# Kernel optimization log

Measured on AMD Instinct MI355X. Metric: run time of the kernel, lower is better.

## Reference

```python
import jax, jax.numpy as jnp
import numpy as np

B, CIN, COUT = 4, 64, 64
D, H, W = 8, 48, 48
KD = KH = KW = 3
K = KD * KH * KW  # 27 sampling taps
STRIDE, PAD, DIL = 1, 1, 1
KOFF, POFF = 3, 1
OFFSET_SCALE = 1.0


def setup_inputs() -> dict:
    key = jax.random.key(0)
    ks = jax.random.split(key, 7)
    x = jax.random.normal(ks[0], (B, CIN, D, H, W), jnp.float32)
    w_off = jax.random.normal(ks[1], (K * 3, CIN, KOFF, KOFF, KOFF), jnp.float32) * 0.01
    b_off = jax.random.normal(ks[2], (K * 3,), jnp.float32) * 0.01
    w_mask = jax.random.normal(ks[3], (K, CIN, KOFF, KOFF, KOFF), jnp.float32) * 0.05
    b_mask = jax.random.normal(ks[4], (K,), jnp.float32) * 0.05
    weight = jax.random.normal(ks[5], (COUT, CIN, KD, KH, KW), jnp.float32) * 0.02
    bias = jax.random.normal(ks[6], (COUT,), jnp.float32) * 0.02
    return dict(x=x, w_off=w_off, b_off=b_off, w_mask=w_mask, b_mask=b_mask,
                weight=weight, bias=bias)


def _conv3d(x, w, b, pad):
    out = jax.lax.conv_general_dilated(
        x, w, window_strides=(1, 1, 1), padding=[(pad, pad)] * 3,
        dimension_numbers=('NCDHW', 'OIDHW', 'NCDHW'))
    return out + b[None, :, None, None, None]


def _trilinear(x_flat, pz, py, px):
    # x_flat: [B, C, N]; pz/py/px: [B, N] fractional positions. Zero padding outside.
    z0, y0, x0 = jnp.floor(pz), jnp.floor(py), jnp.floor(px)
    acc = jnp.zeros_like(x_flat)
    for dz in (0.0, 1.0):
        for dy in (0.0, 1.0):
            for dx in (0.0, 1.0):
                zi, yi, xi = z0 + dz, y0 + dy, x0 + dx
                wgt = ((1.0 - jnp.abs(pz - zi)) * (1.0 - jnp.abs(py - yi))
                       * (1.0 - jnp.abs(px - xi)))
                valid = ((zi >= 0) & (zi < D) & (yi >= 0) & (yi < H)
                         & (xi >= 0) & (xi < W)).astype(x_flat.dtype)
                idx = ((jnp.clip(zi, 0, D - 1) * H + jnp.clip(yi, 0, H - 1)) * W
                       + jnp.clip(xi, 0, W - 1)).astype(jnp.int32)
                g = jnp.take_along_axis(x_flat, idx[:, None, :], axis=2)  # [B,C,N]
                acc = acc + g * (wgt * valid)[:, None, :]
    return acc


def reference(x, w_off, b_off, w_mask, b_mask, weight, bias):
    N = D * H * W
    # learned per-tap 3D offsets: [K, B, 3, N] ordered (dz, dy, dx)
    off = _conv3d(x, w_off, b_off, POFF).reshape(B, K, 3, N)
    off = jnp.transpose(off, (1, 0, 2, 3))
    # DCNv3-style attention mask: softmax over the K taps
    mask = jax.nn.softmax(_conv3d(x, w_mask, b_mask, POFF).reshape(B, K, N), axis=1)
    mask = jnp.transpose(mask, (1, 0, 2))  # [K, B, N]
    zo, yo, xo = jnp.meshgrid(jnp.arange(D, dtype=jnp.float32),
                              jnp.arange(H, dtype=jnp.float32),
                              jnp.arange(W, dtype=jnp.float32), indexing='ij')
    zo, yo, xo = zo.reshape(-1), yo.reshape(-1), xo.reshape(-1)  # [N]
    k_idx = jnp.arange(K)
    kz = (k_idx // (KH * KW)).astype(jnp.float32)
    ky = ((k_idx // KW) % KH).astype(jnp.float32)
    kx = (k_idx % KW).astype(jnp.float32)
    wk = jnp.transpose(weight.reshape(COUT, CIN, K), (2, 0, 1))  # [K, Cout, Cin]
    x_flat = x.reshape(B, CIN, N)

    def step(acc, inp):
        off_k, m_k, kzf, kyf, kxf, w_k = inp
        pz = zo[None] * STRIDE - PAD + kzf * DIL + OFFSET_SCALE * off_k[:, 0]
        py = yo[None] * STRIDE - PAD + kyf * DIL + OFFSET_SCALE * off_k[:, 1]
        px = xo[None] * STRIDE - PAD + kxf * DIL + OFFSET_SCALE * off_k[:, 2]
        s = _trilinear(x_flat, pz, py, px) * m_k[:, None, :]  # [B,Cin,N]
        return acc + jnp.einsum('oi,bin->bon', w_k, s), None

    acc0 = jnp.zeros((B, COUT, N), x.dtype)
    acc, _ = jax.lax.scan(step, acc0, (off, mask, kz, ky, kx, wk))
    return (acc + bias[None, :, None]).reshape(B, COUT, D, H, W)
```

## Files before the change

### kernel.cpp

```cpp
#include <hip/hip_runtime.h>
#include <hip/hip_bf16.h>
#include <math.h>

#define B_    4
#define CIN_  64
#define COUT_ 64
#define DD    8
#define HH    48
#define WW    48
#define HW2   (HH * WW)
#define NN    (DD * HH * WW)
#define BN    (B_ * NN)
#define KK    27
#define RS    116

typedef float f32x2 __attribute__((ext_vector_type(2)));
typedef float f32x4 __attribute__((ext_vector_type(4)));
typedef unsigned int u32x4 __attribute__((ext_vector_type(4)));
typedef __bf16 bf16x8 __attribute__((ext_vector_type(8)));
typedef __hip_bfloat16 bf16_t;

__device__ __forceinline__ float bflo(unsigned int u) {
  return __uint_as_float(u << 16);
}
__device__ __forceinline__ float bfhi(unsigned int u) {
  return __uint_as_float(u & 0xffff0000u);
}

__global__ __launch_bounds__(256) void init_kernel(
    const float* __restrict__ w_off, const float* __restrict__ w_mask,
    const float* __restrict__ weight, bf16_t* __restrict__ wB,
    bf16_t* __restrict__ wBd, bf16_t* __restrict__ zp)
{
  const int o = blockIdx.x * 256 + threadIdx.x;
  {
    const int ci = o & 63;
    const int ch = (o >> 6) % 112;
    const int k  = o / (112 * 64);
    float v = 0.f;
    if (ch < 81)       v = w_off[((size_t)ch * CIN_ + ci) * KK + k];
    else if (ch < 108) v = w_mask[((size_t)(ch - 81) * CIN_ + ci) * KK + k];
    wB[o] = __float2bfloat16(v);
  }
  if (o < KK * CIN_ * COUT_) {
    const int ci = o & 63;
    const int co = (o >> 6) & 63;
    const int k  = o >> 12;
    wBd[o] = __float2bfloat16(weight[((size_t)co * CIN_ + ci) * KK + k]);
  }
  if (o < 128) zp[o] = __float2bfloat16(0.f);
}

__global__ __launch_bounds__(256) void transpose_x_kernel(
    const float* __restrict__ x, bf16_t* __restrict__ xTbf)
{
  const int tid = threadIdx.x;
  const int n0  = blockIdx.x * 64;
  const int b   = blockIdx.y;
  __shared__ float tile[64][65];

  for (int i = tid; i < 4096; i += 256) {
    const int c  = i >> 6;
    const int nl = i & 63;
    tile[c][nl] = x[((size_t)(b * CIN_ + c)) * NN + n0 + nl];
  }
  __syncthreads();
  for (int i = tid; i < 4096; i += 256) {
    const int nl = i >> 6;
    const int c  = i & 63;
    xTbf[((size_t)(b * NN + n0 + nl)) * CIN_ + c] = __float2bfloat16(tile[c][nl]);
  }
}

__global__ __launch_bounds__(128) void fused_kernel(
    const bf16_t* __restrict__ xTbf, const bf16_t* __restrict__ wB,
    const float* __restrict__ b_off, const float* __restrict__ b_mask,
    const bf16_t* __restrict__ zp, const bf16_t* __restrict__ wBd,
    const float* __restrict__ bias, float* __restrict__ out)
{
  const int bid  = (blockIdx.x % 8) * 288 + blockIdx.x / 8;
  const int tid  = threadIdx.x;
  const int wid  = tid >> 6;
  const int lane = tid & 63;
  const int lg   = lane >> 4;
  const int lr   = lane & 15;

  const int b    = bid / 576;
  const int rem  = bid % 576;
  const int z    = rem / 72;
  const int r2   = rem % 72;
  const int y0   = (r2 / 3) * 2;
  const int x0   = (r2 % 3) * 16;
  const int n0   = (z * HH + y0) * WW + x0;

  __shared__ float OM[32][RS];
  __shared__ __align__(16) char SPu[9216];
  unsigned short* Sw  = (unsigned short*)SPu + wid * 2048;
  unsigned int*   SwU = (unsigned int*)Sw;
  float*          Pp  = (float*)SPu;

  const bf16_t* xb = xTbf + (size_t)b * NN * CIN_;

  const int ck0 = wid ? 14 : 0;
  const int ck1 = wid ? 27 : 14;

  f32x4 acc[2][7];
#pragma unroll
  for (int mf = 0; mf < 2; ++mf)
#pragma unroll
    for (int nf = 0; nf < 7; ++nf) acc[mf][nf] = (f32x4){0.f, 0.f, 0.f, 0.f};

#pragma unroll 3
  for (int k = ck0; k < ck1; ++k) {
    const int kz = k / 9;
    const int kr = k - kz * 9;
    const int ky = kr / 3;
    const int kx = kr - ky * 3;

    bf16x8 afr[2][2];
    const int zz = z + kz - 1;
    const int xx = x0 + lr + kx - 1;
    const bool vzx = ((unsigned)zz < (unsigned)DD) & ((unsigned)xx < (unsigned)WW);
#pragma unroll
    for (int mf = 0; mf < 2; ++mf) {
      const int yy = y0 + mf + ky - 1;
      const bool v = vzx & ((unsigned)yy < (unsigned)HH);
      const bf16_t* ab = v ? (xb + (size_t)((zz * HH + yy) * WW + xx) * CIN_) : zp;
      afr[mf][0] = *(const bf16x8*)(ab + 8 * lg);
      afr[mf][1] = *(const bf16x8*)(ab + 32 + 8 * lg);
    }

    const bf16_t* wk = wB + (size_t)k * (112 * 64) + lr * 64 + 8 * lg;
#pragma unroll
    for (int nf = 0; nf < 7; ++nf) {
      const bf16x8 b0 = *(const bf16x8*)(wk + nf * 1024);
      const bf16x8 b1 = *(const bf16x8*)(wk + nf * 1024 + 32);
      acc[0][nf] = __builtin_amdgcn_mfma_f32_16x16x32_bf16(afr[0][0], b0, acc[0][nf], 0, 0, 0);
      acc[1][nf] = __builtin_amdgcn_mfma_f32_16x16x32_bf16(afr[1][0], b0, acc[1][nf], 0, 0, 0);
      acc[0][nf] = __builtin_amdgcn_mfma_f32_16x16x32_bf16(afr[0][1], b1, acc[0][nf], 0, 0, 0);
      acc[1][nf] = __builtin_amdgcn_mfma_f32_16x16x32_bf16(afr[1][1], b1, acc[1][nf], 0, 0, 0);
    }
  }

  if (wid == 0) {
#pragma unroll
    for (int nf = 0; nf < 7; ++nf) {
      const int ch = 16 * nf + lr;
      if (ch < 108) {
        const float bv   = (ch < 81) ? b_off[ch] : b_mask[ch - 81];
        const int   slot = (ch < 81) ? (4 * (ch / 3) + (ch % 3)) : (4 * (ch - 81) + 3);
#pragma unroll
        for (int mf = 0; mf < 2; ++mf)
#pragma unroll
          for (int r = 0; r < 4; ++r)
            OM[mf * 16 + 4 * lg + r][slot] = acc[mf][nf][r] + bv;
      }
    }
  }
  __syncthreads();
  if (wid == 1) {
#pragma unroll
    for (int nf = 0; nf < 7; ++nf) {
      const int ch = 16 * nf + lr;
      if (ch < 108) {
        const int slot = (ch < 81) ? (4 * (ch / 3) + (ch % 3)) : (4 * (ch - 81) + 3);
#pragma unroll
        for (int mf = 0; mf < 2; ++mf)
#pragma unroll
          for (int r = 0; r < 4; ++r)
            OM[mf * 16 + 4 * lg + r][slot] += acc[mf][nf][r];
      }
    }
  }
  __syncthreads();

  if (lane < 16) {
    const int pos = wid * 16 + lane;
    float v[KK];
    float mx = -1e30f;
#pragma unroll
    for (int k = 0; k < KK; ++k) { v[k] = OM[pos][4 * k + 3]; mx = fmaxf(mx, v[k]); }
    float s = 0.f;
#pragma unroll
    for (int k = 0; k < KK; ++k) { v[k] = expf(v[k] - mx); s += v[k]; }
    const float inv = 1.f / s;
#pragma unroll
    for (int k = 0; k < KK; ++k) OM[pos][4 * k + 3] = v[k] * inv;
  }
  __syncthreads();

  const int p8 = lane >> 3;
  const int q  = lane & 7;

  const unsigned short* xq = (const unsigned short*)xb + (q << 3);

  float pxb[4], pyb[4];
#pragma unroll
  for (int oct = 0; oct < 4; ++oct) {
    const int j  = oct * 8 + p8;
    pyb[oct] = (float)(y0 + (j >> 4) - 1);
    pxb[oct] = (float)(x0 + (j & 15) - 1);
  }
  const float pzb = (float)(z - 1);

  const int dk0 = wid ? 14 : 0;
  const int dkN = wid ? 13 : 14;

  f32x4 dacc[2][4];
#pragma unroll
  for (int mf = 0; mf < 2; ++mf)
#pragma unroll
    for (int nf = 0; nf < 4; ++nf) dacc[mf][nf] = (f32x4){0.f, 0.f, 0.f, 0.f};

#pragma unroll 2
  for (int t = 0; t < dkN; ++t) {
    const int k  = dk0 + t;
    const int kz = k / 9;
    const int kr = k - kz * 9;
    const int ky = kr / 3;
    const int kx = kr - ky * 3;
    const float kzf = (float)kz, kyf = (float)ky, kxf = (float)kx;

#pragma unroll
    for (int oct = 0; oct < 4; ++oct) {
      const int j = oct * 8 + p8;
      const f32x4 om = *(const f32x4*)(&OM[j][4 * k]);

      const float pz = pzb + kzf + om.x;
      const float py = pyb[oct] + kyf + om.y;
      const float px = pxb[oct] + kxf + om.z;
      const float m  = om.w;

      const float zf = floorf(pz); const float fz = pz - zf; const int z0 = (int)zf;
      const float yf = floorf(py); const float fy = py - yf; const int y0i = (int)yf;
      const float xf = floorf(px); const float fx = px - xf; const int xi0 = (int)xf;

      const float wz0 = ((unsigned)z0        < DD) ? (1.f - fz) : 0.f;
      const float wz1 = ((unsigned)(z0 + 1)  < DD) ? fz         : 0.f;
      const float wy0 = ((unsigned)y0i       < HH) ? (1.f - fy) : 0.f;
      const float wy1 = ((unsigned)(y0i + 1) < HH) ? fy         : 0.f;
      const float wx0 = ((unsigned)xi0       < WW) ? (1.f - fx) : 0.f;
      const float wx1 = ((unsigned)(xi0 + 1) < WW) ? fx         : 0.f;

      const int z0c = min(max(z0, 0),      DD - 1);
      const int z1c = min(max(z0 + 1, 0),  DD - 1);
      const int y0c = min(max(y0i, 0),     HH - 1);
      const int y1c = min(max(y0i + 1, 0), HH - 1);
      const int x0c = min(max(xi0, 0),     WW - 1);
      const int x1c = min(max(xi0 + 1, 0), WW - 1);

      const int r00 = (z0c * HH + y0c) * WW;
      const int r01 = (z0c * HH + y1c) * WW;
      const int r10 = (z1c * HH + y0c) * WW;
      const int r11 = (z1c * HH + y1c) * WW;

      const int rows[8] = {r00 + x0c, r00 + x1c, r01 + x0c, r01 + x1c,
                           r10 + x0c, r10 + x1c, r11 + x0c, r11 + x1c};
      const float w00 = wz0 * wy0, w01 = wz0 * wy1;
      const float w10 = wz1 * wy0, w11 = wz1 * wy1;
      const float wgt[8] = {w00 * wx0, w00 * wx1, w01 * wx0, w01 * wx1,
                            w10 * wx0, w10 * wx1, w11 * wx0, w11 * wx1};

      u32x4 cv[8];
#pragma unroll
      for (int c = 0; c < 8; ++c)
        cv[c] = *(const u32x4*)(xq + ((size_t)rows[c] << 6));

      f32x2 a01 = {0.f, 0.f}, a23 = {0.f, 0.f}, a45 = {0.f, 0.f}, a67 = {0.f, 0.f};
#pragma unroll
      for (int c = 0; c < 8; ++c) {
        const float w_ = wgt[c];
        a01 += (f32x2){bflo(cv[c].x), bfhi(cv[c].x)} * w_;
        a23 += (f32x2){bflo(cv[c].y), bfhi(cv[c].y)} * w_;
        a45 += (f32x2){bflo(cv[c].z), bfhi(cv[c].z)} * w_;
        a67 += (f32x2){bflo(cv[c].w), bfhi(cv[c].w)} * w_;
      }

      a01 *= m; a23 *= m; a45 *= m; a67 *= m;
      unsigned int d0, d1, d2, d3;
      asm("v_cvt_pk_bf16_f32 %0, %1, %2" : "=v"(d0) : "v"(a01.x), "v"(a01.y));
      asm("v_cvt_pk_bf16_f32 %0, %1, %2" : "=v"(d1) : "v"(a23.x), "v"(a23.y));
      asm("v_cvt_pk_bf16_f32 %0, %1, %2" : "=v"(d2) : "v"(a45.x), "v"(a45.y));
      asm("v_cvt_pk_bf16_f32 %0, %1, %2" : "=v"(d3) : "v"(a67.x), "v"(a67.y));
      const int slot = q ^ (j & 7);
      *(u32x4*)(SwU + j * 32 + slot * 4) = (u32x4){d0, d1, d2, d3};
    }

    bf16x8 afr2[2][2];
#pragma unroll
    for (int mf = 0; mf < 2; ++mf)
#pragma unroll
      for (int t2 = 0; t2 < 2; ++t2) {
        const int row  = 16 * mf + lr;
        const int slot = (t2 * 4 + lg) ^ (row & 7);
        afr2[mf][t2] = *(const bf16x8*)(Sw + row * 64 + slot * 8);
      }
    const bf16_t* wk = wBd + (size_t)k * 4096 + lr * 64 + 8 * lg;
#pragma unroll
    for (int nf = 0; nf < 4; ++nf) {
      const bf16x8 wv0 = *(const bf16x8*)(wk + nf * 1024);
      const bf16x8 wv1 = *(const bf16x8*)(wk + nf * 1024 + 32);
      dacc[0][nf] = __builtin_amdgcn_mfma_f32_16x16x32_bf16(afr2[0][0], wv0, dacc[0][nf], 0, 0, 0);
      dacc[1][nf] = __builtin_amdgcn_mfma_f32_16x16x32_bf16(afr2[1][0], wv0, dacc[1][nf], 0, 0, 0);
      dacc[0][nf] = __builtin_amdgcn_mfma_f32_16x16x32_bf16(afr2[0][1], wv1, dacc[0][nf], 0, 0, 0);
      dacc[1][nf] = __builtin_amdgcn_mfma_f32_16x16x32_bf16(afr2[1][1], wv1, dacc[1][nf], 0, 0, 0);
    }
  }

  __syncthreads();
  if (wid == 1) {
#pragma unroll
    for (int nf = 0; nf < 4; ++nf)
#pragma unroll
      for (int mf = 0; mf < 2; ++mf)
        *(f32x4*)(Pp + (16 * nf + lr) * 36 + 16 * mf + 4 * lg) = dacc[mf][nf];
  }
  __syncthreads();
  if (wid == 0) {
#pragma unroll
    for (int nf = 0; nf < 4; ++nf) {
      const float bv = bias[16 * nf + lr];
      float* op = out + ((size_t)(b * COUT_ + 16 * nf + lr)) * NN + n0 + 4 * lg;
#pragma unroll
      for (int mf = 0; mf < 2; ++mf) {
        const f32x4 p = *(const f32x4*)(Pp + (16 * nf + lr) * 36 + 16 * mf + 4 * lg);
        *(f32x4*)(op + mf * WW) = dacc[mf][nf] + p + bv;
      }
    }
  }
}

extern "C" void kernel_launch(void* const* d_in, const int* in_sizes, int n_in,
                              void* d_out, int out_size, void* d_ws, size_t ws_size,
                              hipStream_t stream)
{
  const float* x      = (const float*)d_in[0];
  const float* w_off  = (const float*)d_in[1];
  const float* b_off  = (const float*)d_in[2];
  const float* w_mask = (const float*)d_in[3];
  const float* b_mask = (const float*)d_in[4];
  const float* weight = (const float*)d_in[5];
  const float* bias   = (const float*)d_in[6];
  float* out = (float*)d_out;

  char* ws = (char*)d_ws;
  bf16_t* xTbf = (bf16_t*)ws;
  bf16_t* wB   = (bf16_t*)(ws + 9437184);
  bf16_t* wBd  = (bf16_t*)(ws + 9824256);
  bf16_t* zp   = (bf16_t*)(ws + 10045440);

  init_kernel<<<(KK * 112 * 64) / 256, 256, 0, stream>>>(w_off, w_mask, weight,
                                                         wB, wBd, zp);
  dim3 gtx(NN / 64, B_);
  transpose_x_kernel<<<gtx, 256, 0, stream>>>(x, xTbf);

  fused_kernel<<<2304, 128, 0, stream>>>(xTbf, wB, b_off, b_mask, zp, wBd,
                                         bias, out);
}
```

Measured before the change: 279.7 us.

## Split kernel taps across four waves per block instead of two

The fused kernel now runs 256 threads (4 waves) per block, and each wave handles about a quarter of the 27 taps in both the offset/mask convolution and the deformable sampling stage. Partial accumulators are reduced serially through shared memory with a barrier per wave, and the softmax is spread over 8 lanes per wave. The aim is more latency hiding and shorter per-wave serial chains per block, at the cost of extra shared memory, more barriers and serialized reductions, which may lower occupancy.

Result: no change. 282.3 us (+0.9%).

```diff
diff --git a/kernel.cpp b/kernel.cpp
--- a/kernel.cpp
+++ b/kernel.cpp
@@ -72,7 +72,7 @@
   }
 }
 
-__global__ __launch_bounds__(128) void fused_kernel(
+__global__ __launch_bounds__(256) void fused_kernel(
     const bf16_t* __restrict__ xTbf, const bf16_t* __restrict__ wB,
     const float* __restrict__ b_off, const float* __restrict__ b_mask,
     const bf16_t* __restrict__ zp, const bf16_t* __restrict__ wBd,
@@ -94,15 +94,15 @@
   const int n0   = (z * HH + y0) * WW + x0;
 
   __shared__ float OM[32][RS];
-  __shared__ __align__(16) char SPu[9216];
+  __shared__ __align__(16) char SPu[16384];
   unsigned short* Sw  = (unsigned short*)SPu + wid * 2048;
   unsigned int*   SwU = (unsigned int*)Sw;
   float*          Pp  = (float*)SPu;
 
   const bf16_t* xb = xTbf + (size_t)b * NN * CIN_;
 
-  const int ck0 = wid ? 14 : 0;
-  const int ck1 = wid ? 27 : 14;
+  const int ck0 = wid * 7;
+  const int ck1 = (wid == 3) ? 27 : (wid * 7 + 7);
 
   f32x4 acc[2][7];
 #pragma unroll
@@ -142,40 +142,31 @@
     }
   }
 
-  if (wid == 0) {
-#pragma unroll
-    for (int nf = 0; nf < 7; ++nf) {
-      const int ch = 16 * nf + lr;
-      if (ch < 108) {
-        const float bv   = (ch < 81) ? b_off[ch] : b_mask[ch - 81];
-        const int   slot = (ch < 81) ? (4 * (ch / 3) + (ch % 3)) : (4 * (ch - 81) + 3);
-#pragma unroll
-        for (int mf = 0; mf < 2; ++mf)
-#pragma unroll
-          for (int r = 0; r < 4; ++r)
-            OM[mf * 16 + 4 * lg + r][slot] = acc[mf][nf][r] + bv;
+#pragma unroll 1
+  for (int w = 0; w < 4; ++w) {
+    if (wid == w) {
+#pragma unroll
+      for (int nf = 0; nf < 7; ++nf) {
+        const int ch = 16 * nf + lr;
+        if (ch < 108) {
+          const float bv   = (ch < 81) ? b_off[ch] : b_mask[ch - 81];
+          const int   slot = (ch < 81) ? (4 * (ch / 3) + (ch % 3)) : (4 * (ch - 81) + 3);
+#pragma unroll
+          for (int mf = 0; mf < 2; ++mf)
+#pragma unroll
+            for (int r = 0; r < 4; ++r) {
+              const int pos = mf * 16 + 4 * lg + r;
+              if (w == 0) OM[pos][slot]  = acc[mf][nf][r] + bv;
+              else        OM[pos][slot] += acc[mf][nf][r];
+            }
+        }
       }
     }
-  }
-  __syncthreads();
-  if (wid == 1) {
-#pragma unroll
-    for (int nf = 0; nf < 7; ++nf) {
-      const int ch = 16 * nf + lr;
-      if (ch < 108) {
-        const int slot = (ch < 81) ? (4 * (ch / 3) + (ch % 3)) : (4 * (ch - 81) + 3);
-#pragma unroll
-        for (int mf = 0; mf < 2; ++mf)
-#pragma unroll
-          for (int r = 0; r < 4; ++r)
-            OM[mf * 16 + 4 * lg + r][slot] += acc[mf][nf][r];
-      }
-    }
-  }
-  __syncthreads();
-
-  if (lane < 16) {
-    const int pos = wid * 16 + lane;
+    __syncthreads();
+  }
+
+  if (lane < 8) {
+    const int pos = wid * 8 + lane;
     float v[KK];
     float mx = -1e30f;
 #pragma unroll
@@ -203,9 +194,6 @@
   }
   const float pzb = (float)(z - 1);
 
-  const int dk0 = wid ? 14 : 0;
-  const int dkN = wid ? 13 : 14;
-
   f32x4 dacc[2][4];
 #pragma unroll
   for (int mf = 0; mf < 2; ++mf)
@@ -213,8 +201,7 @@
     for (int nf = 0; nf < 4; ++nf) dacc[mf][nf] = (f32x4){0.f, 0.f, 0.f, 0.f};
 
 #pragma unroll 2
-  for (int t = 0; t < dkN; ++t) {
-    const int k  = dk0 + t;
+  for (int k = ck0; k < ck1; ++k) {
     const int kz = k / 9;
     const int kr = k - kz * 9;
     const int ky = kr / 3;
@@ -308,14 +295,20 @@
   }
 
   __syncthreads();
-  if (wid == 1) {
-#pragma unroll
-    for (int nf = 0; nf < 4; ++nf)
-#pragma unroll
-      for (int mf = 0; mf < 2; ++mf)
-        *(f32x4*)(Pp + (16 * nf + lr) * 36 + 16 * mf + 4 * lg) = dacc[mf][nf];
-  }
-  __syncthreads();
+#pragma unroll 1
+  for (int w = 1; w < 4; ++w) {
+    if (wid == w) {
+#pragma unroll
+      for (int nf = 0; nf < 4; ++nf)
+#pragma unroll
+        for (int mf = 0; mf < 2; ++mf) {
+          float* pp = Pp + (16 * nf + lr) * 36 + 16 * mf + 4 * lg;
+          if (w == 1) *(f32x4*)pp = dacc[mf][nf];
+          else        *(f32x4*)pp = *(const f32x4*)pp + dacc[mf][nf];
+        }
+    }
+    __syncthreads();
+  }
   if (wid == 0) {
 #pragma unroll
     for (int nf = 0; nf < 4; ++nf) {
@@ -354,6 +347,6 @@
   dim3 gtx(NN / 64, B_);
   transpose_x_kernel<<<gtx, 256, 0, stream>>>(x, xTbf);
 
-  fused_kernel<<<2304, 128, 0, stream>>>(xTbf, wB, b_off, b_mask, zp, wBd,
+  fused_kernel<<<2304, 256, 0, stream>>>(xTbf, wB, b_off, b_mask, zp, wBd,
                                          bias, out);
 }
```

## Precompute trilinear sample descriptors once per position in LDS; raise MFMA priority

Applied to the files above, without the earlier changes.

The deformable sampling loop previously had each of the 8 lanes serving a position recompute the trilinear coordinates, clamps, row offsets and weights for 4 octets. Now pairs of lanes compute descriptors (byte row offset and mask-premultiplied weight) for one position and one z-slice each, and store them in a per-wave LDS table. The gather loop then reads them back, removing redundant address math. s_setprio raises wave priority around the MFMA blocks in both conv phases. In exchange this adds LDS traffic and relies on intra-wave ordering with no barrier between the descriptor writes and reads.

Result: slower. 293.7 us (+5.0%).

```diff
diff --git a/kernel.cpp b/kernel.cpp
--- a/kernel.cpp
+++ b/kernel.cpp
@@ -95,6 +95,7 @@
 
   __shared__ float OM[32][RS];
   __shared__ __align__(16) char SPu[9216];
+  __shared__ __align__(16) unsigned int DESC[2][32][16];
   unsigned short* Sw  = (unsigned short*)SPu + wid * 2048;
   unsigned int*   SwU = (unsigned int*)Sw;
   float*          Pp  = (float*)SPu;
@@ -131,6 +132,7 @@
     }
 
     const bf16_t* wk = wB + (size_t)k * (112 * 64) + lr * 64 + 8 * lg;
+    __builtin_amdgcn_s_setprio(1);
 #pragma unroll
     for (int nf = 0; nf < 7; ++nf) {
       const bf16x8 b0 = *(const bf16x8*)(wk + nf * 1024);
@@ -140,6 +142,7 @@
       acc[0][nf] = __builtin_amdgcn_mfma_f32_16x16x32_bf16(afr[0][1], b1, acc[0][nf], 0, 0, 0);
       acc[1][nf] = __builtin_amdgcn_mfma_f32_16x16x32_bf16(afr[1][1], b1, acc[1][nf], 0, 0, 0);
     }
+    __builtin_amdgcn_s_setprio(0);
   }
 
   if (wid == 0) {
@@ -191,20 +194,16 @@
 
   const int p8 = lane >> 3;
   const int q  = lane & 7;
-
-  const unsigned short* xq = (const unsigned short*)xb + (q << 3);
-
-  float pxb[4], pyb[4];
-#pragma unroll
-  for (int oct = 0; oct < 4; ++oct) {
-    const int j  = oct * 8 + p8;
-    pyb[oct] = (float)(y0 + (j >> 4) - 1);
-    pxb[oct] = (float)(x0 + (j & 15) - 1);
-  }
-  const float pzb = (float)(z - 1);
+  const char* xqc = (const char*)xb + q * 16;
+
+  const int sp = lane >> 1;
+  const int sh = lane & 1;
+  const float spz = (float)(z - 1);
+  const float spy = (float)(y0 + (sp >> 4) - 1);
+  const float spx = (float)(x0 + (sp & 15) - 1);
 
   const int dk0 = wid ? 14 : 0;
-  const int dkN = wid ? 13 : 14;
+  const int dk1 = wid ? 27 : 14;
 
   f32x4 dacc[2][4];
 #pragma unroll
@@ -213,22 +212,17 @@
     for (int nf = 0; nf < 4; ++nf) dacc[mf][nf] = (f32x4){0.f, 0.f, 0.f, 0.f};
 
 #pragma unroll 2
-  for (int t = 0; t < dkN; ++t) {
-    const int k  = dk0 + t;
+  for (int k = dk0; k < dk1; ++k) {
     const int kz = k / 9;
     const int kr = k - kz * 9;
     const int ky = kr / 3;
     const int kx = kr - ky * 3;
-    const float kzf = (float)kz, kyf = (float)ky, kxf = (float)kx;
-
-#pragma unroll
-    for (int oct = 0; oct < 4; ++oct) {
-      const int j = oct * 8 + p8;
-      const f32x4 om = *(const f32x4*)(&OM[j][4 * k]);
-
-      const float pz = pzb + kzf + om.x;
-      const float py = pyb[oct] + kyf + om.y;
-      const float px = pxb[oct] + kxf + om.z;
+
+    {
+      const f32x4 om = *(const f32x4*)(&OM[sp][4 * k]);
+      const float pz = spz + (float)kz + om.x;
+      const float py = spy + (float)ky + om.y;
+      const float px = spx + (float)kx + om.z;
       const float m  = om.w;
 
       const float zf = floorf(pz); const float fz = pz - zf; const int z0 = (int)zf;
@@ -249,22 +243,44 @@
       const int x0c = min(max(xi0, 0),     WW - 1);
       const int x1c = min(max(xi0 + 1, 0), WW - 1);
 
-      const int r00 = (z0c * HH + y0c) * WW;
-      const int r01 = (z0c * HH + y1c) * WW;
-      const int r10 = (z1c * HH + y0c) * WW;
-      const int r11 = (z1c * HH + y1c) * WW;
-
-      const int rows[8] = {r00 + x0c, r00 + x1c, r01 + x0c, r01 + x1c,
-                           r10 + x0c, r10 + x1c, r11 + x0c, r11 + x1c};
-      const float w00 = wz0 * wy0, w01 = wz0 * wy1;
-      const float w10 = wz1 * wy0, w11 = wz1 * wy1;
-      const float wgt[8] = {w00 * wx0, w00 * wx1, w01 * wx0, w01 * wx1,
-                            w10 * wx0, w10 * wx1, w11 * wx0, w11 * wx1};
+      const int   zcs = sh ? z1c : z0c;
+      const float wzs = (sh ? wz1 : wz0) * m;
+      const int   rzb = zcs * HH;
+
+      unsigned int dw[8];
+#pragma unroll
+      for (int cc = 0; cc < 4; ++cc) {
+        const int cy = cc >> 1, cx = cc & 1;
+        const int row = (rzb + (cy ? y1c : y0c)) * WW + (cx ? x1c : x0c);
+        const float wg = wzs * (cy ? wy1 : wy0) * (cx ? wx1 : wx0);
+        dw[2 * cc]     = (unsigned)(row << 7);
+        dw[2 * cc + 1] = __float_as_uint(wg);
+      }
+      unsigned int* dst = &DESC[wid][sp][sh * 8];
+      *(u32x4*)(dst)     = (u32x4){dw[0], dw[1], dw[2], dw[3]};
+      *(u32x4*)(dst + 4) = (u32x4){dw[4], dw[5], dw[6], dw[7]};
+    }
+
+#pragma unroll
+    for (int oct = 0; oct < 4; ++oct) {
+      const int j = oct * 8 + p8;
+      const u32x4* dp = (const u32x4*)(&DESC[wid][j][0]);
+      const u32x4 dA = dp[0], dB = dp[1], dC = dp[2], dD = dp[3];
 
       u32x4 cv[8];
-#pragma unroll
-      for (int c = 0; c < 8; ++c)
-        cv[c] = *(const u32x4*)(xq + ((size_t)rows[c] << 6));
+      cv[0] = *(const u32x4*)(xqc + dA.x);
+      cv[1] = *(const u32x4*)(xqc + dA.z);
+      cv[2] = *(const u32x4*)(xqc + dB.x);
+      cv[3] = *(const u32x4*)(xqc + dB.z);
+      cv[4] = *(const u32x4*)(xqc + dC.x);
+      cv[5] = *(const u32x4*)(xqc + dC.z);
+      cv[6] = *(const u32x4*)(xqc + dD.x);
+      cv[7] = *(const u32x4*)(xqc + dD.z);
+      const float wgt[8] = {
+        __uint_as_float(dA.y), __uint_as_float(dA.w),
+        __uint_as_float(dB.y), __uint_as_float(dB.w),
+        __uint_as_float(dC.y), __uint_as_float(dC.w),
+        __uint_as_float(dD.y), __uint_as_float(dD.w)};
 
       f32x2 a01 = {0.f, 0.f}, a23 = {0.f, 0.f}, a45 = {0.f, 0.f}, a67 = {0.f, 0.f};
 #pragma unroll
@@ -276,7 +292,6 @@
         a67 += (f32x2){bflo(cv[c].w), bfhi(cv[c].w)} * w_;
       }
 
-      a01 *= m; a23 *= m; a45 *= m; a67 *= m;
       unsigned int d0, d1, d2, d3;
       asm("v_cvt_pk_bf16_f32 %0, %1, %2" : "=v"(d0) : "v"(a01.x), "v"(a01.y));
       asm("v_cvt_pk_bf16_f32 %0, %1, %2" : "=v"(d1) : "v"(a23.x), "v"(a23.y));
@@ -296,6 +311,7 @@
         afr2[mf][t2] = *(const bf16x8*)(Sw + row * 64 + slot * 8);
       }
     const bf16_t* wk = wBd + (size_t)k * 4096 + lr * 64 + 8 * lg;
+    __builtin_amdgcn_s_setprio(1);
 #pragma unroll
     for (int nf = 0; nf < 4; ++nf) {
       const bf16x8 wv0 = *(const bf16x8*)(wk + nf * 1024);
@@ -305,6 +321,7 @@
       dacc[0][nf] = __builtin_amdgcn_mfma_f32_16x16x32_bf16(afr2[0][1], wv1, dacc[0][nf], 0, 0, 0);
       dacc[1][nf] = __builtin_amdgcn_mfma_f32_16x16x32_bf16(afr2[1][1], wv1, dacc[1][nf], 0, 0, 0);
     }
+    __builtin_amdgcn_s_setprio(0);
   }
 
   __syncthreads();
```
